# Kernel optimization log

Measured on AMD Instinct MI355X. Metric: run time of the kernel, lower is better.

Reference implementation:

```python
import jax, jax.numpy as jnp
import numpy as np

B = 8192
IN = 2048
H = 2048


def setup_inputs() -> dict:
    key = jax.random.key(0)
    ks = jax.random.split(key, 6)
    stdv = 1.0 / np.sqrt(H)
    return {
        "x": jax.random.normal(ks[0], (B, IN), dtype=jnp.float32),
        "h_prev": jax.random.normal(ks[1], (B, H), dtype=jnp.float32),
        "c_prev": jax.random.normal(ks[2], (B, H), dtype=jnp.float32),
        "weight_ih": jax.random.normal(ks[3], (4 * H, IN), dtype=jnp.float32) * stdv,
        "weight_hh": jax.random.normal(ks[4], (4 * H, H), dtype=jnp.float32) * stdv,
        "bias": jax.random.normal(ks[5], (4 * H,), dtype=jnp.float32) * stdv,
    }


def reference(x, h_prev, c_prev, weight_ih, weight_hh, bias):
    # gates: [B, 4H] = x @ W_ih^T + h_prev @ W_hh^T + b
    gates = x @ weight_ih.T + h_prev @ weight_hh.T + bias
    i, f, j, o = jnp.split(gates, 4, axis=1)
    i = jax.nn.sigmoid(i)
    f = jax.nn.sigmoid(f)
    o = jax.nn.sigmoid(o)
    j = jnp.tanh(j)
    # cap_input_gate=True: input gate capped by (1 - f)
    c = f * c_prev + jnp.minimum(1.0 - f, i) * j
    h = o * jnp.tanh(c)
    return (h, c)
```

## Files before the change

### kernel.cpp

```cpp
#include <hip/hip_runtime.h>

#define DEVI __device__ __forceinline__

typedef __attribute__((ext_vector_type(8))) __bf16 bf16x8;
typedef __attribute__((ext_vector_type(16))) float floatx16;

constexpr int Bsz = 8192;
constexpr int Hd  = 2048;
constexpr int INd = 2048;
constexpr int N1  = Bsz * INd;

DEVI unsigned short f2bf_rne(float f) {
  unsigned int u = __float_as_uint(f);
  u += 0x7FFFu + ((u >> 16) & 1u);
  return (unsigned short)(u >> 16);
}

__global__ void cvt4(const float* __restrict__ s0, const float* __restrict__ s1,
                     const float* __restrict__ s2, const float* __restrict__ s3,
                     unsigned short* __restrict__ dst) {
  const float* src = (blockIdx.y == 0) ? s0 : (blockIdx.y == 1) ? s1
                   : (blockIdx.y == 2) ? s2 : s3;
  unsigned short* out = dst + (size_t)blockIdx.y * N1;
  const int nv = N1 / 4;
  for (int i = blockIdx.x * blockDim.x + threadIdx.x; i < nv;
       i += gridDim.x * blockDim.x) {
    float4 v = ((const float4*)src)[i];
    ushort4 o;
    o.x = f2bf_rne(v.x); o.y = f2bf_rne(v.y);
    o.z = f2bf_rne(v.z); o.w = f2bf_rne(v.w);
    ((ushort4*)out)[i] = o;
  }
}

DEVI void gload_lds16(const void* g, void* l) {
  __builtin_amdgcn_global_load_lds(
      (const __attribute__((address_space(1))) void*)g,
      (__attribute__((address_space(3))) void*)l, 16, 0, 0);
}

DEVI float sigm(float x) { return 1.0f / (1.0f + __expf(-x)); }

__global__ __launch_bounds__(512, 2) void lstm_gemm(
    const unsigned short* __restrict__ ws,
    const float* __restrict__ bias,
    const float* __restrict__ c_prev,
    float* __restrict__ out_h,
    float* __restrict__ out_c) {
  __shared__ __align__(16) unsigned short sm[4 * 256 * 64];
  char* smc = (char*)sm;

  const unsigned short* xb  = ws;
  const unsigned short* hb  = ws + (size_t)N1;
  const unsigned short* wih = ws + (size_t)2 * N1;
  const unsigned short* whh = ws + (size_t)3 * N1;

  const int tid  = threadIdx.x;
  const int lane = tid & 63;
  const int wid  = tid >> 6;
  const int ww   = wid >> 2;
  const int wb   = wid & 3;
  const int l31  = lane & 31, l5 = lane >> 5;
  const int lr8  = lane >> 3;
  const int swc  = ((lane & 7) ^ lr8) * 8;

  const int wg = blockIdx.x;
  const int x8 = wg & 7;
  const int lc = wg >> 3;
  const int bc = (x8 & 3) * 8 + (lc & 7);
  const int rb = ((x8 >> 2) * 16 + (lc >> 3)) * 256;

  unsigned int aOff[2][2], bOff[2][2];
#pragma unroll
  for (int h = 0; h < 2; ++h)
#pragma unroll
    for (int j = 0; j < 2; ++j) {
      const int arow = rb + h * 128 + j * 64 + wid * 8 + lr8;
      aOff[h][j] = (unsigned)arow * 2048u + (unsigned)swc;
      const int wr = h * 128 + j * 64 + wid * 8 + lr8;
      const int wrow = ((wr >> 3) & 3) * 2048 + bc * 64 + (wr >> 5) * 8 + (wr & 7);
      bOff[h][j] = (unsigned)wrow * 2048u + (unsigned)swc;
    }

  floatx16 acc[2][2][2];
#pragma unroll
  for (int a = 0; a < 2; ++a)
#pragma unroll
    for (int b = 0; b < 2; ++b)
#pragma unroll
      for (int c = 0; c < 2; ++c)
#pragma unroll
        for (int e = 0; e < 16; ++e) acc[a][b][c][e] = 0.f;

#define STAGE_A(ts, h) {                                                      \
    const int bs_ = (ts) & 1;                                                 \
    const unsigned short* s_ = (((ts) < 32) ? xb : hb) + (((ts) & 31) * 64);  \
    gload_lds16(s_ + aOff[h][0], smc + bs_ * 32768 + ((h) * 128 + wid * 8) * 128);        \
    gload_lds16(s_ + aOff[h][1], smc + bs_ * 32768 + ((h) * 128 + 64 + wid * 8) * 128); }
#define STAGE_B(ts, h) {                                                      \
    const int bs_ = (ts) & 1;                                                 \
    const unsigned short* s_ = (((ts) < 32) ? wih : whh) + (((ts) & 31) * 64);\
    gload_lds16(s_ + bOff[h][0], smc + 65536 + bs_ * 32768 + ((h) * 128 + wid * 8) * 128);        \
    gload_lds16(s_ + bOff[h][1], smc + 65536 + bs_ * 32768 + ((h) * 128 + 64 + wid * 8) * 128); }

#define LDW(DST, QW)                                                          \
  _Pragma("unroll") for (int mrw = 0; mrw < 2; ++mrw)                         \
    _Pragma("unroll") for (int ks = 0; ks < 4; ++ks) {                        \
      const int row  = (QW) * 128 + ww * 64 + mrw * 32 + l31;                 \
      const int phys = (ks * 2 + l5) ^ (row & 7);                             \
      DST[mrw][ks] = *(const bf16x8*)(Bb + row * 128 + phys * 16); }
#define LDX(DST, QB)                                                          \
  _Pragma("unroll") for (int ks = 0; ks < 4; ++ks) {                          \
      const int row  = (QB) * 128 + wb * 32 + l31;                            \
      const int phys = (ks * 2 + l5) ^ (row & 7);                             \
      DST[ks] = *(const bf16x8*)(Ab + row * 128 + phys * 16); }
#define MM(QW, QB, WF, XF)                                                    \
  __builtin_amdgcn_s_setprio(1);                                              \
  _Pragma("unroll") for (int mrw = 0; mrw < 2; ++mrw)                         \
    _Pragma("unroll") for (int ks = 0; ks < 4; ++ks)                          \
      acc[QW][mrw][QB] = __builtin_amdgcn_mfma_f32_32x32x16_bf16(             \
          WF[mrw][ks], XF[ks], acc[QW][mrw][QB], 0, 0, 0);                    \
  __builtin_amdgcn_s_setprio(0);
#define BAR  asm volatile("s_barrier" ::: "memory")
#define VM4  asm volatile("s_waitcnt vmcnt(4)" ::: "memory")
#define VM0  asm volatile("s_waitcnt vmcnt(0)" ::: "memory")
#define NOP  (void)0

#define KTILE(BETA, S1, S2a, S2b, S3, W4) {                                   \
    const char* Ab = smc + (BETA) * 32768;                                    \
    const char* Bb = smc + 65536 + (BETA) * 32768;                            \
    bf16x8 wf[2][4], xf0[4], xf1[4];                                          \
    LDW(wf, 0); LDX(xf0, 0); S1;                                              \
    MM(0, 0, wf, xf0); BAR;                                                   \
    LDX(xf1, 1); S2a; S2b;                                                    \
    MM(0, 1, wf, xf1); BAR;                                                   \
    LDW(wf, 1); S3;                                                           \
    MM(1, 1, wf, xf1); BAR;                                                   \
    LDX(xf0, 0);                                                              \
    MM(1, 0, wf, xf0); W4; BAR;                                               \
  }

  STAGE_A(0, 0); STAGE_A(0, 1); STAGE_B(0, 0); STAGE_B(0, 1);
  STAGE_B(1, 0); STAGE_A(1, 1);
  VM4;
  BAR;

  for (int t = 0; t < 62; ++t) {
    KTILE(t & 1, STAGE_A(t + 1, 0), STAGE_B(t + 1, 1),
          STAGE_B(t + 2, 0), STAGE_A(t + 2, 1), VM4);
  }
  KTILE(0, STAGE_A(63, 0), STAGE_B(63, 1), NOP, NOP, VM0);
  KTILE(1, NOP, NOP, NOP, NOP, NOP);

#pragma unroll
  for (int qw = 0; qw < 2; ++qw)
#pragma unroll
    for (int mrw = 0; mrw < 2; ++mrw) {
      const int hb4 = bc * 64 + (qw * 4 + ww * 2 + mrw) * 8 + l5 * 4;
      const float4 bi4 = *(const float4*)&bias[hb4];
      const float4 bf4 = *(const float4*)&bias[2048 + hb4];
      const float4 bj4 = *(const float4*)&bias[4096 + hb4];
      const float4 bo4 = *(const float4*)&bias[6144 + hb4];
#pragma unroll
      for (int qb = 0; qb < 2; ++qb) {
        const int brow = rb + qb * 128 + wb * 32 + l31;
        const size_t base = (size_t)brow * 2048 + hb4;
        const float4 cp = *(const float4*)&c_prev[base];
        float4 hv, cv;
#pragma unroll
        for (int q = 0; q < 4; ++q) {
          const float gi = acc[qw][mrw][qb][q]      + ((const float*)&bi4)[q];
          const float gf = acc[qw][mrw][qb][4 + q]  + ((const float*)&bf4)[q];
          const float gj = acc[qw][mrw][qb][8 + q]  + ((const float*)&bj4)[q];
          const float go = acc[qw][mrw][qb][12 + q] + ((const float*)&bo4)[q];
          const float iv = sigm(gi);
          const float fv = sigm(gf);
          const float jv = tanhf(gj);
          const float ov = sigm(go);
          const float cq = fv * ((const float*)&cp)[q] + fminf(1.0f - fv, iv) * jv;
          ((float*)&cv)[q] = cq;
          ((float*)&hv)[q] = ov * tanhf(cq);
        }
        *(float4*)&out_h[base] = hv;
        *(float4*)&out_c[base] = cv;
      }
    }
}

extern "C" void kernel_launch(void* const* d_in, const int* in_sizes, int n_in,
                              void* d_out, int out_size, void* d_ws, size_t ws_size,
                              hipStream_t stream) {
  const float* x      = (const float*)d_in[0];
  const float* h_prev = (const float*)d_in[1];
  const float* c_prev = (const float*)d_in[2];
  const float* w_ih   = (const float*)d_in[3];
  const float* w_hh   = (const float*)d_in[4];
  const float* bias   = (const float*)d_in[5];

  float* out_h = (float*)d_out;
  float* out_c = out_h + (size_t)Bsz * Hd;
  unsigned short* wsb = (unsigned short*)d_ws;

  dim3 cgrid(2048, 4);
  cvt4<<<cgrid, 256, 0, stream>>>(x, h_prev, w_ih, w_hh, wsb);

  lstm_gemm<<<1024, 512, 0, stream>>>(wsb, bias, c_prev, out_h, out_c);
}
```

Before: 640.0 us.

## Use K-major LDS layout with per-lane row loads, reorder MFMA schedule, fast tanh

Changes the LDS staging layout so each lane loads one row's 16-byte chunk per wave-assigned k-slice, giving a k-major layout that MFMA fragment reads hit with simple precomputed pointer offsets instead of XOR swizzles. The per-tile schedule is reordered to load both W fragment sets and reuse x fragments, cutting barriers from four to two per k-tile, and the loop is unrolled by two so buffer parity is compile-time. The epilogue also replaces tanhf with an exp-based tanh. Risks include LDS bank conflicts from the unswizzled layout, higher register pressure from holding two W fragment sets, and possible overwrite hazards from fewer barriers.

```diff
diff --git a/kernel.cpp b/kernel.cpp
--- a/kernel.cpp
+++ b/kernel.cpp
@@ -40,6 +40,7 @@
 }
 
 DEVI float sigm(float x) { return 1.0f / (1.0f + __expf(-x)); }
+DEVI float tanh_fast(float x) { return 1.0f - 2.0f / (1.0f + __expf(2.0f * x)); }
 
 __global__ __launch_bounds__(512, 2) void lstm_gemm(
     const unsigned short* __restrict__ ws,
@@ -47,7 +48,7 @@
     const float* __restrict__ c_prev,
     float* __restrict__ out_h,
     float* __restrict__ out_c) {
-  __shared__ __align__(16) unsigned short sm[4 * 256 * 64];
+  __shared__ __align__(16) unsigned short sm[2 * 2 * 256 * 64];
   char* smc = (char*)sm;
 
   const unsigned short* xb  = ws;
@@ -61,8 +62,6 @@
   const int ww   = wid >> 2;
   const int wb   = wid & 3;
   const int l31  = lane & 31, l5 = lane >> 5;
-  const int lr8  = lane >> 3;
-  const int swc  = ((lane & 7) ^ lr8) * 8;
 
   const int wg = blockIdx.x;
   const int x8 = wg & 7;
@@ -70,17 +69,23 @@
   const int bc = (x8 & 3) * 8 + (lc & 7);
   const int rb = ((x8 >> 2) * 16 + (lc >> 3)) * 256;
 
-  unsigned int aOff[2][2], bOff[2][2];
-#pragma unroll
-  for (int h = 0; h < 2; ++h)
-#pragma unroll
-    for (int j = 0; j < 2; ++j) {
-      const int arow = rb + h * 128 + j * 64 + wid * 8 + lr8;
-      aOff[h][j] = (unsigned)arow * 2048u + (unsigned)swc;
-      const int wr = h * 128 + j * 64 + wid * 8 + lr8;
-      const int wrow = ((wr >> 3) & 3) * 2048 + bc * 64 + (wr >> 5) * 8 + (wr & 7);
-      bOff[h][j] = (unsigned)wrow * 2048u + (unsigned)swc;
-    }
+  unsigned int aOff[4], bOff[4];
+#pragma unroll
+  for (int j = 0; j < 4; ++j) {
+    const int arow = rb + j * 64 + lane;
+    aOff[j] = (unsigned)arow * 2048u + (unsigned)(wid * 8);
+    const int wr = j * 64 + lane;
+    const int wrow = ((wr >> 3) & 3) * 2048 + bc * 64 + (wr >> 5) * 8 + (wr & 7);
+    bOff[j] = (unsigned)wrow * 2048u + (unsigned)(wid * 8);
+  }
+
+  const char* pX[2];
+  const char* pW[2];
+#pragma unroll
+  for (int p = 0; p < 2; ++p) {
+    pX[p] = smc + p * 65536 + wb * 512 + l31 * 16 + l5 * 4096;
+    pW[p] = smc + p * 65536 + 32768 + ww * 1024 + l31 * 16 + l5 * 4096;
+  }
 
   floatx16 acc[2][2][2];
 #pragma unroll
@@ -93,27 +98,23 @@
         for (int e = 0; e < 16; ++e) acc[a][b][c][e] = 0.f;
 
 #define STAGE_A(ts, h) {                                                      \
-    const int bs_ = (ts) & 1;                                                 \
+    const int p_ = (ts) & 1;                                                  \
     const unsigned short* s_ = (((ts) < 32) ? xb : hb) + (((ts) & 31) * 64);  \
-    gload_lds16(s_ + aOff[h][0], smc + bs_ * 32768 + ((h) * 128 + wid * 8) * 128);        \
-    gload_lds16(s_ + aOff[h][1], smc + bs_ * 32768 + ((h) * 128 + 64 + wid * 8) * 128); }
+    gload_lds16(s_ + aOff[2 * (h)],     smc + p_ * 65536 + wid * 4096 + (2 * (h)) * 1024);     \
+    gload_lds16(s_ + aOff[2 * (h) + 1], smc + p_ * 65536 + wid * 4096 + (2 * (h) + 1) * 1024); }
 #define STAGE_B(ts, h) {                                                      \
-    const int bs_ = (ts) & 1;                                                 \
+    const int p_ = (ts) & 1;                                                  \
     const unsigned short* s_ = (((ts) < 32) ? wih : whh) + (((ts) & 31) * 64);\
-    gload_lds16(s_ + bOff[h][0], smc + 65536 + bs_ * 32768 + ((h) * 128 + wid * 8) * 128);        \
-    gload_lds16(s_ + bOff[h][1], smc + 65536 + bs_ * 32768 + ((h) * 128 + 64 + wid * 8) * 128); }
-
-#define LDW(DST, QW)                                                          \
+    gload_lds16(s_ + bOff[2 * (h)],     smc + p_ * 65536 + 32768 + wid * 4096 + (2 * (h)) * 1024);     \
+    gload_lds16(s_ + bOff[2 * (h) + 1], smc + p_ * 65536 + 32768 + wid * 4096 + (2 * (h) + 1) * 1024); }
+
+#define LDW(D, P, QW)                                                         \
   _Pragma("unroll") for (int mrw = 0; mrw < 2; ++mrw)                         \
-    _Pragma("unroll") for (int ks = 0; ks < 4; ++ks) {                        \
-      const int row  = (QW) * 128 + ww * 64 + mrw * 32 + l31;                 \
-      const int phys = (ks * 2 + l5) ^ (row & 7);                             \
-      DST[mrw][ks] = *(const bf16x8*)(Bb + row * 128 + phys * 16); }
-#define LDX(DST, QB)                                                          \
-  _Pragma("unroll") for (int ks = 0; ks < 4; ++ks) {                          \
-      const int row  = (QB) * 128 + wb * 32 + l31;                            \
-      const int phys = (ks * 2 + l5) ^ (row & 7);                             \
-      DST[ks] = *(const bf16x8*)(Ab + row * 128 + phys * 16); }
+    _Pragma("unroll") for (int ks = 0; ks < 4; ++ks)                          \
+      D[mrw][ks] = *(const bf16x8*)(pW[P] + ((QW) * 2048 + mrw * 512 + ks * 8192));
+#define LDX(D, P, QB)                                                         \
+  _Pragma("unroll") for (int ks = 0; ks < 4; ++ks)                            \
+      D[ks] = *(const bf16x8*)(pX[P] + ((QB) * 2048 + ks * 8192));
 #define MM(QW, QB, WF, XF)                                                    \
   __builtin_amdgcn_s_setprio(1);                                              \
   _Pragma("unroll") for (int mrw = 0; mrw < 2; ++mrw)                         \
@@ -126,28 +127,28 @@
 #define VM0  asm volatile("s_waitcnt vmcnt(0)" ::: "memory")
 #define NOP  (void)0
 
-#define KTILE(BETA, S1, S2a, S2b, S3, W4) {                                   \
-    const char* Ab = smc + (BETA) * 32768;                                    \
-    const char* Bb = smc + 65536 + (BETA) * 32768;                            \
-    bf16x8 wf[2][4], xf0[4], xf1[4];                                          \
-    LDW(wf, 0); LDX(xf0, 0); S1;                                              \
-    MM(0, 0, wf, xf0); BAR;                                                   \
-    LDX(xf1, 1); S2a; S2b;                                                    \
-    MM(0, 1, wf, xf1); BAR;                                                   \
-    LDW(wf, 1); S3;                                                           \
-    MM(1, 1, wf, xf1); BAR;                                                   \
-    LDX(xf0, 0);                                                              \
-    MM(1, 0, wf, xf0); W4; BAR;                                               \
-  }
-
-  STAGE_A(0, 0); STAGE_A(0, 1); STAGE_B(0, 0); STAGE_B(0, 1);
+#define KTILE(P, S1, S2a, S2b, S3, W4) {                                      \
+    bf16x8 w0[2][4], w1[2][4], x0[4], x1[4];                                  \
+    LDW(w0, P, 0); LDX(x0, P, 0); S1;                                         \
+    MM(0, 0, w0, x0);                                                         \
+    LDW(w1, P, 1); S2a;                                                       \
+    MM(1, 0, w1, x0); BAR;                                                    \
+    LDX(x1, P, 1); S2b; S3;                                                   \
+    MM(1, 1, w1, x1);                                                         \
+    MM(0, 1, w0, x1); W4; BAR;                                                \
+  }
+
+  STAGE_A(0, 0); STAGE_B(0, 0); STAGE_A(0, 1); STAGE_B(0, 1);
   STAGE_B(1, 0); STAGE_A(1, 1);
-  VM4;
+  VM0;
   BAR;
 
-  for (int t = 0; t < 62; ++t) {
-    KTILE(t & 1, STAGE_A(t + 1, 0), STAGE_B(t + 1, 1),
-          STAGE_B(t + 2, 0), STAGE_A(t + 2, 1), VM4);
+  for (int u = 0; u < 31; ++u) {
+    const int t0 = 2 * u;
+    KTILE(0, STAGE_A(t0 + 1, 0), STAGE_B(t0 + 1, 1),
+          STAGE_B(t0 + 2, 0), STAGE_A(t0 + 2, 1), VM4);
+    KTILE(1, STAGE_A(t0 + 2, 0), STAGE_B(t0 + 2, 1),
+          STAGE_B(t0 + 3, 0), STAGE_A(t0 + 3, 1), VM4);
   }
   KTILE(0, STAGE_A(63, 0), STAGE_B(63, 1), NOP, NOP, VM0);
   KTILE(1, NOP, NOP, NOP, NOP, NOP);
@@ -175,11 +176,11 @@
           const float go = acc[qw][mrw][qb][12 + q] + ((const float*)&bo4)[q];
           const float iv = sigm(gi);
           const float fv = sigm(gf);
-          const float jv = tanhf(gj);
+          const float jv = tanh_fast(gj);
           const float ov = sigm(go);
           const float cq = fv * ((const float*)&cp)[q] + fminf(1.0f - fv, iv) * jv;
           ((float*)&cv)[q] = cq;
-          ((float*)&hv)[q] = ov * tanhf(cq);
+          ((float*)&hv)[q] = ov * tanh_fast(cq);
         }
         *(float4*)&out_h[base] = hv;
         *(float4*)&out_c[base] = cv;
```

Measured after the change: 761.5 us. +19.0%, slower.
